# Optimization experiments

Measured on AMD Instinct MI355X. Metric: run time of the kernel, lower is better.

The kernel has to match this reference:

```python
import jax, jax.numpy as jnp
import numpy as np

EPS = 1e-5

def layer_norm(x, g, b):
    m = x.mean(-1, keepdims=True)
    v = ((x - m) ** 2).mean(-1, keepdims=True)
    return (x - m) / jnp.sqrt(v + EPS) * g + b

def lstm(x_sbd, W_ih, W_hh, b_ih, b_hh):
    # x_sbd: (S, B, D); PyTorch gate order i, f, g, o
    S, B, D = x_sbd.shape
    H = W_hh.shape[1]
    h0 = jnp.zeros((B, H), x_sbd.dtype)
    c0 = jnp.zeros((B, H), x_sbd.dtype)
    def step(carry, x_t):
        h, c = carry
        gates = x_t @ W_ih.T + b_ih + h @ W_hh.T + b_hh
        i, f, g, o = jnp.split(gates, 4, axis=-1)
        c = jax.nn.sigmoid(f) * c + jax.nn.sigmoid(i) * jnp.tanh(g)
        h = jax.nn.sigmoid(o) * jnp.tanh(c)
        return (h, c), h
    (hL, _), hs = jax.lax.scan(step, (h0, c0), x_sbd)
    return hs, hL  # (S,B,H), (B,H)

def setup_inputs():
    key = jax.random.key(0)
    ks = jax.random.split(key, 20)
    B, S, D, V = 64, 1024, 128, 50000
    sc = 1.0 / np.sqrt(D)
    r = lambda k, shp, s=sc: (jax.random.normal(k, shp, jnp.float32) * s)
    return {
        "new_list": jax.random.randint(ks[0], (B, S), 0, V, jnp.int32),
        "new_mask": jnp.ones((B, S), jnp.float32),
        "aspect": jax.random.randint(ks[1], (B, 1), 0, V, jnp.int32),
        "gpunum": 0,
        "emb": r(ks[2], (V, D), 0.02),
        "W_ih": r(ks[3], (4 * D, D)),
        "W_hh": r(ks[4], (4 * D, D)),
        "b_ih": jnp.zeros((4 * D,), jnp.float32),
        "b_hh": jnp.zeros((4 * D,), jnp.float32),
        "an_g": jnp.ones((D,), jnp.float32),
        "an_b": jnp.zeros((D,), jnp.float32),
        "hn_g": jnp.ones((D,), jnp.float32),
        "hn_b": jnp.zeros((D,), jnp.float32),
        "W_att": r(ks[5], (D, D)),
        "W_aw": r(ks[6], (1, D)),
        "W_rout": r(ks[7], (D, D)),
        "W_hout": r(ks[8], (D, D)),
        "W_cls": r(ks[9], (2, D)),
        "b_cls": jnp.zeros((2,), jnp.float32),
    }

def reference(new_list, new_mask, aspect, gpunum, emb, W_ih, W_hh, b_ih, b_hh,
              an_g, an_b, hn_g, hn_b, W_att, W_aw, W_rout, W_hout, W_cls, b_cls):
    # embed, seq-major for LSTM
    x = emb[new_list.T]                      # (S, B, D)
    hidden_output, h_L = lstm(x, W_ih, W_hh, b_ih, b_hh)
    aspect_emb = emb[aspect]                 # (B, 1, D)
    aspect_emb = layer_norm(aspect_emb, an_g, an_b)
    hidden_output = layer_norm(hidden_output, hn_g, hn_b)
    hid = jnp.transpose(hidden_output, (1, 0, 2))  # (B, S, D)
    # circular convolution along hidden dim via FFT (batched; replaces host scipy loop)
    M = jnp.real(jnp.fft.ifft(jnp.fft.fft(hid, axis=-1) * jnp.fft.fft(aspect_emb, axis=-1), axis=-1)).astype(hid.dtype)
    # self-attention: key=M, value=hid, mask applied before softmax (as in original)
    QK = jnp.tanh(M @ W_att.T)               # (B, S, D)
    QK = new_mask[..., None] * QK
    weight = jax.nn.softmax(QK @ W_aw.T, axis=1)  # (B, S, 1)
    r = jnp.einsum('bs,bsd->bd', weight[..., 0], hid)
    r = jnp.tanh(r @ W_rout.T + h_L @ W_hout.T)
    result = jax.nn.softmax(r @ W_cls.T + b_cls, axis=-1)
    return (result, r)
```

## Files before the change

### kernel.cpp

```cpp
#include <hip/hip_runtime.h>

typedef __attribute__((ext_vector_type(8))) short s16x8;
typedef __attribute__((ext_vector_type(4))) float f32x4;
typedef __attribute__((ext_vector_type(4))) unsigned short u16x4;
typedef __attribute__((ext_vector_type(8))) unsigned short u16x8;

#define PAD 136

__device__ __forceinline__ unsigned short f2bf(float f){
  union{float f;unsigned u;} v; v.f=f;
  unsigned r=v.u + 0x7fffu + ((v.u>>16)&1u);
  return (unsigned short)(r>>16);
}
__device__ __forceinline__ float bf2f(unsigned short u){
  union{unsigned u;float f;} v; v.u=((unsigned)u)<<16; return v.f;
}
__device__ __forceinline__ float ubits2f(unsigned u){
  union{unsigned u;float f;} v; v.u=u; return v.f;
}
__device__ __forceinline__ float rcp_(float x){ return __builtin_amdgcn_rcpf(x); }
__device__ __forceinline__ float e2_(float x){ return __builtin_amdgcn_exp2f(x); }
__device__ __forceinline__ float tanh_(float x){ return 1.f-2.f*rcp_(1.f+e2_(x*2.885390082f)); }

__device__ __forceinline__ void mfma128(const unsigned short* As, const unsigned short* Bs, f32x4 acc[4][2]){
  const int tid=threadIdx.x, w=tid>>6, l=tid&63;
  const int wm=w>>2, wn=w&3, lr=l&15, lk=(l>>4)*8;
#pragma unroll
  for(int kc=0;kc<4;++kc){
    const int ko=kc*32+lk;
    s16x8 a[4], bb[2];
#pragma unroll
    for(int mt=0;mt<4;++mt) a[mt]=*(const s16x8*)(As+(wm*64+mt*16+lr)*PAD+ko);
#pragma unroll
    for(int nt=0;nt<2;++nt) bb[nt]=*(const s16x8*)(Bs+(wn*32+nt*16+lr)*PAD+ko);
#pragma unroll
    for(int mt=0;mt<4;++mt)
#pragma unroll
      for(int nt=0;nt<2;++nt)
        acc[mt][nt]=__builtin_amdgcn_mfma_f32_16x16x32_bf16(a[mt],bb[nt],acc[mt][nt],0,0,0);
  }
}

__global__ __launch_bounds__(256) void k_cvt(const float* __restrict__ w, unsigned short* __restrict__ o, int n){
  int i = blockIdx.x*256 + threadIdx.x;
  if (i<n) o[i] = f2bf(w[i]);
}

__global__ __launch_bounds__(512) void k_aspg(const int* __restrict__ aspect, const float* __restrict__ emb,
    const float* __restrict__ ang, const float* __restrict__ anb, const float* __restrict__ watt,
    unsigned short* __restrict__ gt){
  __shared__ unsigned short As[128*PAD];
  __shared__ unsigned short Bs[128*PAD];
  __shared__ float a_ln[128];
  __shared__ float stat[2];
  const int b=blockIdx.x, tid=threadIdx.x;
  if (tid<128) a_ln[tid] = emb[(size_t)aspect[b]*128 + tid];
  __syncthreads();
  if (tid==0){
    float s=0.f,q=0.f;
    for(int d=0;d<128;++d){ float v=a_ln[d]; s+=v; q+=v*v; }
    float m=s*(1.f/128.f);
    stat[0]=m; stat[1]=__builtin_amdgcn_rsqf(q*(1.f/128.f)-m*m+1e-5f);
  }
  __syncthreads();
  if (tid<128) a_ln[tid] = (a_ln[tid]-stat[0])*stat[1]*ang[tid]+anb[tid];
  __syncthreads();
  {
    int k=tid>>2, dq=(tid&3)*32;
    for(int d=dq; d<dq+32; ++d) As[k*PAD+d]=f2bf(a_ln[(d-k)&127]);
  }
  {
    int i=tid>>2, kq=(tid&3)*32;
    const f32x4* src=(const f32x4*)(watt+(size_t)i*128+kq);
#pragma unroll
    for(int j=0;j<8;++j){ f32x4 v=src[j]; u16x4 o;
#pragma unroll
      for(int q=0;q<4;++q) o[q]=f2bf(v[q]);
      *(u16x4*)(Bs+i*PAD+kq+4*j)=o; }
  }
  __syncthreads();
  f32x4 z={0.f,0.f,0.f,0.f};
  f32x4 acc[4][2]={{z,z},{z,z},{z,z},{z,z}};
  mfma128(As,Bs,acc);
  const int w=tid>>6,l=tid&63,wm=w>>2,wn=w&3,lr=l&15,lg=l>>4;
#pragma unroll
  for(int mt=0;mt<4;++mt)
#pragma unroll
    for(int nt=0;nt<2;++nt){
      int k0=wm*64+mt*16+lg*4;
      int n=wn*32+nt*16+lr;
      u16x4 o;
#pragma unroll
      for(int r=0;r<4;++r) o[r]=f2bf(acc[mt][nt][r]);
      *(u16x4*)(gt+(size_t)b*16384+n*128+k0)=o;
    }
}

__global__ __launch_bounds__(512) void k_xw(const int* __restrict__ new_list, const float* __restrict__ emb,
    const float* __restrict__ wih, const float* __restrict__ bih, const float* __restrict__ bhh,
    unsigned short* __restrict__ xw){
  __shared__ unsigned short As[128*PAD];
  __shared__ unsigned short Bs[128*PAD];
  const int tid=threadIdx.x;
  const int m0=blockIdx.x*128, n0=blockIdx.y*128;
  {
    int i=tid>>2, kq=(tid&3)*32;
    int m=m0+i, t=m>>6, b=m&63;
    int tok=new_list[b*1024+t];
    const f32x4* src=(const f32x4*)(emb+(size_t)tok*128+kq);
#pragma unroll
    for(int j=0;j<8;++j){ f32x4 v=src[j]; u16x4 o;
#pragma unroll
      for(int q=0;q<4;++q) o[q]=f2bf(v[q]);
      *(u16x4*)(As+i*PAD+kq+4*j)=o; }
  }
  {
    int i=tid>>2, kq=(tid&3)*32;
    const f32x4* src=(const f32x4*)(wih+(size_t)(n0+i)*128+kq);
#pragma unroll
    for(int j=0;j<8;++j){ f32x4 v=src[j]; u16x4 o;
#pragma unroll
      for(int q=0;q<4;++q) o[q]=f2bf(v[q]);
      *(u16x4*)(Bs+i*PAD+kq+4*j)=o; }
  }
  __syncthreads();
  f32x4 z={0.f,0.f,0.f,0.f};
  f32x4 acc[4][2]={{z,z},{z,z},{z,z},{z,z}};
  mfma128(As,Bs,acc);
  const int w=tid>>6,l=tid&63,wm=w>>2,wn=w&3,lr=l&15,lg=l>>4;
#pragma unroll
  for(int nt=0;nt<2;++nt){
    int n=n0+wn*32+nt*16+lr;
    float bias=bih[n]+bhh[n];
#pragma unroll
    for(int mt=0;mt<4;++mt){
      int m_=m0+wm*64+mt*16+lg*4;
      int t=m_>>6, b0=m_&63;
      u16x4 o;
#pragma unroll
      for(int r=0;r<4;++r) o[r]=f2bf(acc[mt][nt][r]+bias);
      *(u16x4*)(xw+(((size_t)t*16+(b0>>2))*512+n)*4)=o;
    }
  }
}

__global__ __launch_bounds__(512) void k_lstm(const unsigned short* __restrict__ xw,
    const unsigned short* __restrict__ whh,
    unsigned short* __restrict__ hraw, float* __restrict__ hL){
  __shared__ unsigned short hbuf[2][4*PAD];
  const int tid=threadIdx.x, w=tid>>6, l=tid&63, lr=l&15, lg=l>>4;
  const int blk=blockIdx.x, bb=blk*4;
  const int cb=w*16+lr;
  s16x8 wf[4][4];
#pragma unroll
  for(int g=0;g<4;++g)
#pragma unroll
    for(int kc=0;kc<4;++kc)
      wf[g][kc]=*(const s16x8*)(whh+(size_t)(g*128+cb)*128+kc*32+lg*8);
  for(int i=tid;i<2*4*PAD;i+=512) ((unsigned short*)hbuf)[i]=0;
  __syncthreads();
  const unsigned short* xwt = xw + (size_t)blk*2048;
  int xofs[4];
#pragma unroll
  for(int g=0;g<4;++g) xofs[g]=((g*128+cb)<<2)+lg;
  unsigned short px[4];
#pragma unroll
  for(int g=0;g<4;++g) px[g]=xwt[xofs[g]];
  unsigned short* hrp=hraw+((size_t)(bb+lg)<<17)+cb;
  float cc=0.f, hh=0.f;
  int cur=0;
  const float L2E=1.442695041f;
  for(int t=0;t<1024;++t){
    const unsigned short* hc=hbuf[cur];
    s16x8 af[4];
#pragma unroll
    for(int kc=0;kc<4;++kc) af[kc]=*(const s16x8*)(hc+(lr&3)*PAD+kc*32+lg*8);
    xwt+=32768;
    unsigned short pn[4];
#pragma unroll
    for(int g=0;g<4;++g) pn[g]=xwt[xofs[g]];
    f32x4 z={0.f,0.f,0.f,0.f};
    f32x4 acc[4]={z,z,z,z};
#pragma unroll
    for(int kc=0;kc<4;++kc)
#pragma unroll
      for(int g=0;g<4;++g)
        acc[g]=__builtin_amdgcn_mfma_f32_16x16x32_bf16(af[kc],wf[g][kc],acc[g],0,0,0);
    float ga[4];
#pragma unroll
    for(int g=0;g<4;++g){
      float s01=(lg&1)?acc[g][1]:acc[g][0];
      float s23=(lg&1)?acc[g][3]:acc[g][2];
      float a=(lg&2)?s23:s01;
      ga[g]=a+ubits2f(((unsigned)px[g])<<16);
      px[g]=pn[g];
    }
    {
      float gg=__builtin_amdgcn_fmed3f(ga[2],-30.f,30.f);
      float ei=e2_(ga[0]*-L2E), eg=e2_(gg*(-2.f*L2E));
      float sitg=rcp_((1.f+ei)*(1.f+eg))*(1.f-eg);
      float sf=rcp_(1.f+e2_(ga[1]*-L2E));
      cc=fmaf(sf,cc,sitg);
      float cl=__builtin_amdgcn_fmed3f(cc,-30.f,30.f);
      float E=e2_(cl*(2.f*L2E)), eo=e2_(ga[3]*-L2E);
      hh=(E-1.f)*rcp_((1.f+eo)*(E+1.f));
    }
    unsigned p;
    asm("v_cvt_pk_bf16_f32 %0, %1, %2":"=v"(p):"v"(hh),"v"(hh));
    unsigned short hb=(unsigned short)(p&0xffffu);
    hbuf[cur^1][lg*PAD+cb]=hb;
    hrp[(size_t)t<<7]=hb;
    __syncthreads();
    cur^=1;
  }
  hL[(size_t)(bb+lg)*128+cb]=hh;
}

__global__ __launch_bounds__(512) void k_scores(const unsigned short* __restrict__ hraw,
    const unsigned short* __restrict__ gt, const float* __restrict__ hng, const float* __restrict__ hnb,
    const float* __restrict__ waw, const float* __restrict__ mask,
    unsigned short* __restrict__ hln, float* __restrict__ scores){
  __shared__ unsigned short As[128*PAD];
  __shared__ unsigned short Bs[128*PAD];
  __shared__ float redS[128][4];
  __shared__ float redQ[128][4];
  __shared__ float red[128][4];
  const int b=blockIdx.x>>3, s0=(blockIdx.x&7)*128;
  const int tid=threadIdx.x;
  const int i=tid>>2, kq=(tid&3)*32;
  u16x8 hv[4];
  {
    const u16x8* src=(const u16x8*)(hraw+((size_t)b*1024+s0+i)*128+kq);
    float s=0.f,q=0.f;
#pragma unroll
    for(int j=0;j<4;++j){ hv[j]=src[j];
#pragma unroll
      for(int e=0;e<8;++e){ float x=bf2f(hv[j][e]); s+=x; q+=x*x; } }
    redS[i][tid&3]=s; redQ[i][tid&3]=q;
  }
  {
    const u16x4* src=(const u16x4*)(gt+(size_t)b*16384+i*128+kq);
#pragma unroll
    for(int j=0;j<8;++j) *(u16x4*)(Bs+i*PAD+kq+4*j)=src[j];
  }
  __syncthreads();
  {
    float s=redS[i][0]+redS[i][1]+redS[i][2]+redS[i][3];
    float q=redQ[i][0]+redQ[i][1]+redQ[i][2]+redQ[i][3];
    float m=s*(1.f/128.f);
    float inv=__builtin_amdgcn_rsqf(q*(1.f/128.f)-m*m+1e-5f);
    unsigned short* dst=hln+((size_t)b*1024+s0+i)*128+kq;
#pragma unroll
    for(int j=0;j<4;++j){ u16x8 o;
#pragma unroll
      for(int e=0;e<8;++e){ int d=kq+j*8+e;
        float x=(bf2f(hv[j][e])-m)*inv*hng[d]+hnb[d];
        o[e]=f2bf(x); }
      *(u16x8*)(As+i*PAD+kq+8*j)=o;
      *(u16x8*)(dst+8*j)=o;
    }
  }
  __syncthreads();
  f32x4 z={0.f,0.f,0.f,0.f};
  f32x4 acc[4][2]={{z,z},{z,z},{z,z},{z,z}};
  mfma128(As,Bs,acc);
  const int w=tid>>6,l=tid&63,wm=w>>2,wn=w&3,lr=l&15,lg=l>>4;
  const float w0=waw[wn*32+lr], w1=waw[wn*32+16+lr];
#pragma unroll
  for(int mt=0;mt<4;++mt){
    f32x4 p4;
#pragma unroll
    for(int r=0;r<4;++r) p4[r]=tanh_(acc[mt][0][r])*w0+tanh_(acc[mt][1][r])*w1;
#pragma unroll
    for(int m=1;m<16;m<<=1){
#pragma unroll
      for(int r=0;r<4;++r) p4[r]+=__shfl_xor(p4[r],m,64);
    }
    if (lr==0){
#pragma unroll
      for(int r=0;r<4;++r) red[wm*64+mt*16+lg*4+r][wn]=p4[r];
    }
  }
  __syncthreads();
  if (tid<128){
    float sc=red[tid][0]+red[tid][1]+red[tid][2]+red[tid][3];
    sc*=mask[b*1024+s0+tid];
    scores[b*1024+s0+tid]=sc;
  }
}

__global__ __launch_bounds__(256) void k_wsum(const float* __restrict__ scores,
    const unsigned short* __restrict__ hln, float* __restrict__ rpre){
  __shared__ float wl[1024];
  __shared__ float red[256];
  __shared__ float part[8][32];
  const int b=blockIdx.x>>2, d0=(blockIdx.x&3)*32;
  const int tid=threadIdx.x;
  float v[4]; float lm=-1e30f;
#pragma unroll
  for(int q=0;q<4;++q){ v[q]=scores[b*1024+tid+256*q]; lm=fmaxf(lm,v[q]); }
  red[tid]=lm; __syncthreads();
  for(int st=128;st;st>>=1){ if(tid<st) red[tid]=fmaxf(red[tid],red[tid+st]); __syncthreads(); }
  const float mx=red[0]; __syncthreads();
  float ls=0.f;
#pragma unroll
  for(int q=0;q<4;++q){ v[q]=e2_((v[q]-mx)*1.442695041f); ls+=v[q]; }
  red[tid]=ls; __syncthreads();
  for(int st=128;st;st>>=1){ if(tid<st) red[tid]+=red[tid+st]; __syncthreads(); }
  const float inv=rcp_(red[0]);
#pragma unroll
  for(int q=0;q<4;++q) wl[tid+256*q]=v[q]*inv;
  __syncthreads();
  const int d=tid&31, sg=tid>>5;
  float acc=0.f;
  const unsigned short* hp=hln+(size_t)b*131072+d0+d;
  for(int s=sg*128;s<sg*128+128;++s) acc+=wl[s]*bf2f(hp[(size_t)s*128]);
  part[sg][d]=acc; __syncthreads();
  if (tid<32){
    float a=0.f;
#pragma unroll
    for(int g=0;g<8;++g) a+=part[g][tid];
    rpre[b*128+d0+tid]=a;
  }
}

__global__ __launch_bounds__(128) void k_final(const float* __restrict__ rpre, const float* __restrict__ hLp,
    const float* __restrict__ wrout, const float* __restrict__ whout, const float* __restrict__ wcls,
    const float* __restrict__ bcls, float* __restrict__ out){
  __shared__ float rv[128], hv[128], cred[4];
  const int b=blockIdx.x, n=threadIdx.x;
  rv[n]=rpre[b*128+n]; hv[n]=hLp[b*128+n];
  __syncthreads();
  float a=0.f;
  const float* wr=wrout+(size_t)n*128;
  const float* wh=whout+(size_t)n*128;
  for(int k=0;k<128;++k) a+=rv[k]*wr[k]+hv[k]*wh[k];
  const float rr=tanh_(a);
  out[128+b*128+n]=rr;
  float p0=rr*wcls[n], p1=rr*wcls[128+n];
#pragma unroll
  for(int m=1;m<64;m<<=1){ p0+=__shfl_xor(p0,m,64); p1+=__shfl_xor(p1,m,64); }
  if ((n&63)==0){ cred[(n>>6)*2]=p0; cred[(n>>6)*2+1]=p1; }
  __syncthreads();
  if (n==0){
    float l0=cred[0]+cred[2]+bcls[0], l1=cred[1]+cred[3]+bcls[1];
    float m=fmaxf(l0,l1);
    float e0=e2_((l0-m)*1.442695041f), e1=e2_((l1-m)*1.442695041f);
    float s=rcp_(e0+e1);
    out[b*2]=e0*s; out[b*2+1]=e1*s;
  }
}

extern "C" void kernel_launch(void* const* d_in, const int* in_sizes, int n_in,
                              void* d_out, int out_size, void* d_ws, size_t ws_size,
                              hipStream_t stream) {
  (void)in_sizes; (void)n_in; (void)out_size; (void)ws_size;
  const int*   new_list=(const int*)d_in[0];
  const float* new_mask=(const float*)d_in[1];
  const int*   aspect  =(const int*)d_in[2];
  const float* emb   =(const float*)d_in[4];
  const float* W_ih  =(const float*)d_in[5];
  const float* W_hh  =(const float*)d_in[6];
  const float* b_ih  =(const float*)d_in[7];
  const float* b_hh  =(const float*)d_in[8];
  const float* an_g  =(const float*)d_in[9];
  const float* an_b  =(const float*)d_in[10];
  const float* hn_g  =(const float*)d_in[11];
  const float* hn_b  =(const float*)d_in[12];
  const float* W_att =(const float*)d_in[13];
  const float* W_aw  =(const float*)d_in[14];
  const float* W_rout=(const float*)d_in[15];
  const float* W_hout=(const float*)d_in[16];
  const float* W_cls =(const float*)d_in[17];
  const float* b_cls =(const float*)d_in[18];
  float* out=(float*)d_out;
  char* ws=(char*)d_ws;
  unsigned short* xw    =(unsigned short*)(ws);
  unsigned short* hraw  =(unsigned short*)(ws+67108864);
  unsigned short* hln   =(unsigned short*)(ws+83886080);
  unsigned short* gt    =(unsigned short*)(ws+100663296);
  unsigned short* whh   =(unsigned short*)(ws+102760448);
  float*          scores=(float*)(ws+102891520);
  float*          hLb   =(float*)(ws+103153664);
  float*          rpre  =(float*)(ws+103186432);
  k_cvt   <<<dim3(256),    dim3(256), 0, stream>>>(W_hh, whh, 512*128);
  k_aspg  <<<dim3(64),     dim3(512), 0, stream>>>(aspect, emb, an_g, an_b, W_att, gt);
  k_xw    <<<dim3(512,4),  dim3(512), 0, stream>>>(new_list, emb, W_ih, b_ih, b_hh, xw);
  k_lstm  <<<dim3(16),     dim3(512), 0, stream>>>(xw, whh, hraw, hLb);
  k_scores<<<dim3(512),    dim3(512), 0, stream>>>(hraw, gt, hn_g, hn_b, W_aw, new_mask, hln, scores);
  k_wsum  <<<dim3(256),    dim3(256), 0, stream>>>(scores, hln, rpre);
  k_final <<<dim3(64),     dim3(128), 0, stream>>>(rpre, hLb, W_rout, W_hout, W_cls, b_cls, out);
}
```

Before: 695.7 us.

## Streamline LSTM recurrence: lighter barrier, deeper gate prefetch, replicated h rows

Replaces __syncthreads in the per-timestep LSTM loop with an explicit LDS-only wait plus s_barrier. This avoids waiting on the outstanding global store of h each step. The precomputed input-gate values are now prefetched two timesteps ahead instead of one, hiding more global-load latency. The A-fragment row mapping is changed so each batch row is replicated across four MFMA rows, which lets lanes read accumulator element 0 directly and drops the select logic; the LDS row pad also grows to 144. The risk is that correctness relies on the global stores to hraw not needing ordering inside the loop.

```diff
diff --git a/kernel.cpp b/kernel.cpp
--- a/kernel.cpp
+++ b/kernel.cpp
@@ -6,6 +6,7 @@
 typedef __attribute__((ext_vector_type(8))) unsigned short u16x8;
 
 #define PAD 136
+#define LPAD 144
 
 __device__ __forceinline__ unsigned short f2bf(float f){
   union{float f;unsigned u;} v; v.f=f;
@@ -147,7 +148,7 @@
 __global__ __launch_bounds__(512) void k_lstm(const unsigned short* __restrict__ xw,
     const unsigned short* __restrict__ whh,
     unsigned short* __restrict__ hraw, float* __restrict__ hL){
-  __shared__ unsigned short hbuf[2][4*PAD];
+  __shared__ unsigned short hbuf[2][4*LPAD];
   const int tid=threadIdx.x, w=tid>>6, l=tid&63, lr=l&15, lg=l>>4;
   const int blk=blockIdx.x, bb=blk*4;
   const int cb=w*16+lr;
@@ -157,15 +158,17 @@
 #pragma unroll
     for(int kc=0;kc<4;++kc)
       wf[g][kc]=*(const s16x8*)(whh+(size_t)(g*128+cb)*128+kc*32+lg*8);
-  for(int i=tid;i<2*4*PAD;i+=512) ((unsigned short*)hbuf)[i]=0;
-  __syncthreads();
-  const unsigned short* xwt = xw + (size_t)blk*2048;
+  for(int i=tid;i<2*4*LPAD;i+=512) ((unsigned short*)hbuf)[i]=0;
+  __syncthreads();
+  const unsigned short* x0 = xw + (size_t)blk*2048;
   int xofs[4];
 #pragma unroll
   for(int g=0;g<4;++g) xofs[g]=((g*128+cb)<<2)+lg;
-  unsigned short px[4];
-#pragma unroll
-  for(int g=0;g<4;++g) px[g]=xwt[xofs[g]];
+  unsigned short px[4], p1[4];
+#pragma unroll
+  for(int g=0;g<4;++g) px[g]=x0[xofs[g]];
+#pragma unroll
+  for(int g=0;g<4;++g) p1[g]=x0[32768+xofs[g]];
   unsigned short* hrp=hraw+((size_t)(bb+lg)<<17)+cb;
   float cc=0.f, hh=0.f;
   int cur=0;
@@ -174,28 +177,25 @@
     const unsigned short* hc=hbuf[cur];
     s16x8 af[4];
 #pragma unroll
-    for(int kc=0;kc<4;++kc) af[kc]=*(const s16x8*)(hc+(lr&3)*PAD+kc*32+lg*8);
-    xwt+=32768;
-    unsigned short pn[4];
-#pragma unroll
-    for(int g=0;g<4;++g) pn[g]=xwt[xofs[g]];
-    f32x4 z={0.f,0.f,0.f,0.f};
-    f32x4 acc[4]={z,z,z,z};
-#pragma unroll
-    for(int kc=0;kc<4;++kc)
-#pragma unroll
-      for(int g=0;g<4;++g)
-        acc[g]=__builtin_amdgcn_mfma_f32_16x16x32_bf16(af[kc],wf[g][kc],acc[g],0,0,0);
-    float ga[4];
-#pragma unroll
-    for(int g=0;g<4;++g){
-      float s01=(lg&1)?acc[g][1]:acc[g][0];
-      float s23=(lg&1)?acc[g][3]:acc[g][2];
-      float a=(lg&2)?s23:s01;
-      ga[g]=a+ubits2f(((unsigned)px[g])<<16);
-      px[g]=pn[g];
-    }
-    {
+    for(int kc=0;kc<4;++kc) af[kc]=*(const s16x8*)(hc+(lr>>2)*LPAD+kc*32+lg*8);
+    { int t2=t+2<1024?t+2:1023;
+      const unsigned short* xq=x0+(size_t)t2*32768;
+      unsigned short pn[4];
+#pragma unroll
+      for(int g=0;g<4;++g) pn[g]=xq[xofs[g]];
+      f32x4 z={0.f,0.f,0.f,0.f};
+      f32x4 acc[4]={z,z,z,z};
+#pragma unroll
+      for(int kc=0;kc<4;++kc)
+#pragma unroll
+        for(int g=0;g<4;++g)
+          acc[g]=__builtin_amdgcn_mfma_f32_16x16x32_bf16(af[kc],wf[g][kc],acc[g],0,0,0);
+      float ga[4];
+#pragma unroll
+      for(int g=0;g<4;++g){
+        ga[g]=acc[g][0]+ubits2f(((unsigned)px[g])<<16);
+        px[g]=p1[g]; p1[g]=pn[g];
+      }
       float gg=__builtin_amdgcn_fmed3f(ga[2],-30.f,30.f);
       float ei=e2_(ga[0]*-L2E), eg=e2_(gg*(-2.f*L2E));
       float sitg=rcp_((1.f+ei)*(1.f+eg))*(1.f-eg);
@@ -208,9 +208,9 @@
     unsigned p;
     asm("v_cvt_pk_bf16_f32 %0, %1, %2":"=v"(p):"v"(hh),"v"(hh));
     unsigned short hb=(unsigned short)(p&0xffffu);
-    hbuf[cur^1][lg*PAD+cb]=hb;
+    hbuf[cur^1][lg*LPAD+cb]=hb;
     hrp[(size_t)t<<7]=hb;
-    __syncthreads();
+    asm volatile("s_waitcnt lgkmcnt(0)\n\ts_barrier" ::: "memory");
     cur^=1;
   }
   hL[(size_t)(bb+lg)*128+cb]=hh;
```

Result: faster. 578.7 us (median of 2 runs) (-16.8%).
